# Performance work log

Measured on AMD Instinct MI355X. Metric: run time of the kernel, lower is better.

## Reference

```python
import jax, jax.numpy as jnp
import numpy as np

D_IN = 1024
D_OUT = 1024
N, S = 4, 2048

def setup_inputs() -> dict:
    key = jax.random.key(0)
    kv, kk, kq, k1, k2, k3 = jax.random.split(key, 6)
    return {
        "v": jax.random.normal(kv, (N, S, D_IN), dtype=jnp.float32),
        "k": jax.random.normal(kk, (N, S, D_IN), dtype=jnp.float32),
        "q": jax.random.normal(kq, (N, S, D_IN), dtype=jnp.float32),
        "WV": jax.random.normal(k1, (D_OUT, D_IN), dtype=jnp.float32),
        "WQ": jax.random.normal(k2, (D_OUT, D_IN), dtype=jnp.float32),
        "WK": jax.random.normal(k3, (D_OUT, D_IN), dtype=jnp.float32),
    }

def reference(v, k, q, WV, WQ, WK) -> jnp.ndarray:
    # projections: x @ W.T  -> [N, S, D_OUT]
    wv = jnp.einsum('nsw,ow->nso', v, WV)
    wk = jnp.einsum('nsw,ow->nso', k, WK)
    wq = jnp.einsum('nsw,ow->nso', q, WQ)
    # scores [N, Sq, Sk]; NOTE: softmax over axis=1 (query axis, matching torch dim=1),
    # then post-hoc division by input_shape[0] AFTER softmax (faithful to source).
    scores = jnp.einsum('nqo,nko->nqk', wq, wk)
    wqk = jax.nn.softmax(scores, axis=1) / jnp.float32(D_IN)
    return jnp.einsum('nqk,nko->nqo', wqk, wv)
```

## Files before the change

kernel.cpp:

```cpp
#include <hip/hip_runtime.h>
#include <math.h>


typedef _Float16 f16;
typedef _Float16 f16x8 __attribute__((ext_vector_type(8)));
typedef float f32x4 __attribute__((ext_vector_type(4)));

enum StageMode { SM_F32SPLIT, SM_F32HI, SM_PLANES2, SM_PLANES1, SM_EXP };
enum EpiMode   { EPI_F32, EPI_SPLIT, EPI_F16T };

#define PAD_PITCH 40
#define GLL_PITCH 32

__device__ __forceinline__ void gll16(const f16* g, f16* l) {
    __builtin_amdgcn_global_load_lds(
        (const __attribute__((address_space(1))) void*)g,
        (__attribute__((address_space(3))) void*)l, 16, 0, 0);
}

__device__ __forceinline__ void stage_gll_plane(const f16* __restrict__ gplane,
                                                f16* __restrict__ lds,
                                                long rowBase, int ld, int k0,
                                                int wave, int lane)
{
#pragma unroll
    for (int i = 0; i < 2; i++) {
        int slotBase = (wave * 2 + i) * 64;
        int t = slotBase + lane;
        int r = t >> 2;
        int c = (t & 3) ^ ((r >> 1) & 3);
        const f16* g = gplane + (rowBase + r) * (long)ld + k0 + c * 8;
        gll16(g, lds + (long)slotBase * 8);
    }
}

__device__ __forceinline__ int frag_off_gll(int row, int g) {
    return row * GLL_PITCH + ((g ^ ((row >> 1) & 3)) << 3);
}
__device__ __forceinline__ int frag_off_pad(int row, int g) {
    return row * PAD_PITCH + (g << 3);
}

template<StageMode SM>
__device__ __forceinline__ void stage_f32_tile(const float* __restrict__ gf,
                                               const float* __restrict__ pM,
                                               const float* __restrict__ pR,
                                               f16* __restrict__ Shi, f16* __restrict__ Slo,
                                               long rowBase, int ld, int k0, int tid)
{
#pragma unroll
    for (int i = 0; i < 2; i++) {
        int c  = tid + i * 256;
        int r  = c >> 2;
        int cc = c & 3;
        long g = (rowBase + r) * (long)ld + k0 + cc * 8;
        float4 x0 = *(const float4*)&gf[g];
        float4 x1 = *(const float4*)&gf[g + 4];
        float xs[8] = {x0.x, x0.y, x0.z, x0.w, x1.x, x1.y, x1.z, x1.w};
        if constexpr (SM == SM_EXP) {
            float4 ma = *(const float4*)&pM[k0 + cc * 8];
            float4 mb = *(const float4*)&pM[k0 + cc * 8 + 4];
            float4 ra = *(const float4*)&pR[k0 + cc * 8];
            float4 rb = *(const float4*)&pR[k0 + cc * 8 + 4];
            float ms[8] = {ma.x, ma.y, ma.z, ma.w, mb.x, mb.y, mb.z, mb.w};
            float rs[8] = {ra.x, ra.y, ra.z, ra.w, rb.x, rb.y, rb.z, rb.w};
            f16x8 h;
#pragma unroll
            for (int e = 0; e < 8; e++)
                h[e] = (f16)(__expf(xs[e] - ms[e]) * rs[e]);
            *(f16x8*)&Shi[r * PAD_PITCH + cc * 8] = h;
        } else if constexpr (SM == SM_F32HI) {
            f16x8 h;
#pragma unroll
            for (int e = 0; e < 8; e++) h[e] = (f16)xs[e];
            *(f16x8*)&Shi[r * PAD_PITCH + cc * 8] = h;
        } else {
            f16x8 h, l;
#pragma unroll
            for (int e = 0; e < 8; e++) {
                f16 hh = (f16)xs[e];
                h[e] = hh;
                l[e] = (f16)(xs[e] - (float)hh);
            }
            *(f16x8*)&Shi[r * PAD_PITCH + cc * 8] = h;
            *(f16x8*)&Slo[r * PAD_PITCH + cc * 8] = l;
        }
    }
}

template<StageMode SA, StageMode SB, EpiMode EP, int GROUPM, bool STATS>
__global__ __launch_bounds__(256, 4)
void mfma_gemm(const void* __restrict__ Ahi, const void* __restrict__ Alo,
               const void* __restrict__ Bhi, const void* __restrict__ Blo,
               const float* __restrict__ statM, const float* __restrict__ statR,
               float* __restrict__ pmOut, float* __restrict__ psOut,
               void* __restrict__ C0, void* __restrict__ C1,
               int M, int Nc, int K, int lda, int ldb, int ldc,
               long batchA, long batchB, long batchC,
               float epiScale, int tsShift)
{
    constexpr bool TRIPLE = (SA == SM_F32SPLIT || SA == SM_PLANES2);
    constexpr bool A_GLL  = (SA == SM_PLANES2 || SA == SM_PLANES1);
    constexpr bool B_GLL  = (SB == SM_PLANES2 || SB == SM_PLANES1);
    constexpr int A_SZ = A_GLL ? 128 * GLL_PITCH : 128 * PAD_PITCH;
    constexpr int B_SZ = B_GLL ? 128 * GLL_PITCH : 128 * PAD_PITCH;

    int bx, by;
    if constexpr (GROUPM > 0) {
        int gx = gridDim.x;
        int lin = blockIdx.y * gx + blockIdx.x;
        int nig = GROUPM * gx;
        int gid = lin / nig;
        int rem = lin - gid * nig;
        by = gid * GROUPM + (rem % GROUPM);
        bx = rem / GROUPM;
    } else {
        bx = blockIdx.x;
        by = blockIdx.y;
    }
    const int n0 = bx * 128;
    const int m0 = by * 128;
    const long z = blockIdx.z;

    long aOfs = z * batchA, bOfs = z * batchB, cOfs = z * batchC;
    const float* pM = statM + z * (long)K;
    const float* pR = statR + z * (long)K;

    __shared__ __align__(16) f16 As_hi[A_SZ];
    __shared__ __align__(16) f16 Bs_hi[B_SZ];
    __shared__ __align__(16) f16 As_lo[TRIPLE ? A_SZ : 8];
    __shared__ __align__(16) f16 Bs_lo[TRIPLE ? B_SZ : 8];

    const int tid  = threadIdx.x;
    const int lane = tid & 63;
    const int wave = tid >> 6;
    const int wr = (wave >> 1) * 64;
    const int wc = (wave & 1) * 64;
    const int fm = lane & 15;
    const int fg = lane >> 4;
    const int fk = fg * 8;

    f32x4 acc[4][4];
#pragma unroll
    for (int i = 0; i < 4; i++)
#pragma unroll
        for (int j = 0; j < 4; j++) acc[i][j] = (f32x4){0.f, 0.f, 0.f, 0.f};

    int roA[4], roB[4];
#pragma unroll
    for (int i = 0; i < 4; i++) {
        int rowA = wr + i * 16 + fm;
        int rowB = wc + i * 16 + fm;
        roA[i] = A_GLL ? frag_off_gll(rowA, fg) : frag_off_pad(rowA, fg);
        roB[i] = B_GLL ? frag_off_gll(rowB, fg) : frag_off_pad(rowB, fg);
    }

    for (int k0 = 0; k0 < K; k0 += 32) {
        if constexpr (SA == SM_PLANES2) {
            stage_gll_plane((const f16*)Ahi + aOfs, As_hi, m0, lda, k0, wave, lane);
            stage_gll_plane((const f16*)Alo + aOfs, As_lo, m0, lda, k0, wave, lane);
        } else if constexpr (SA == SM_PLANES1) {
            stage_gll_plane((const f16*)Ahi + aOfs, As_hi, m0, lda, k0, wave, lane);
        } else {
            stage_f32_tile<SA>((const float*)Ahi + aOfs, pM, pR, As_hi, As_lo, m0, lda, k0, tid);
        }
        if constexpr (SB == SM_PLANES2) {
            stage_gll_plane((const f16*)Bhi + bOfs, Bs_hi, n0, ldb, k0, wave, lane);
            stage_gll_plane((const f16*)Blo + bOfs, Bs_lo, n0, ldb, k0, wave, lane);
        } else if constexpr (SB == SM_PLANES1) {
            stage_gll_plane((const f16*)Bhi + bOfs, Bs_hi, n0, ldb, k0, wave, lane);
        } else {
            stage_f32_tile<SB>((const float*)Bhi + bOfs, nullptr, nullptr, Bs_hi, Bs_lo, n0, ldb, k0, tid);
        }
        __syncthreads();

        f16x8 ah[4], bh[4], al[4], bl[4];
#pragma unroll
        for (int i = 0; i < 4; i++) {
            ah[i] = *(const f16x8*)&As_hi[roA[i]];
            bh[i] = *(const f16x8*)&Bs_hi[roB[i]];
            if constexpr (TRIPLE) {
                al[i] = *(const f16x8*)&As_lo[roA[i]];
                bl[i] = *(const f16x8*)&Bs_lo[roB[i]];
            }
        }
#pragma unroll
        for (int i = 0; i < 4; i++) {
#pragma unroll
            for (int j = 0; j < 4; j++) {
                acc[i][j] = __builtin_amdgcn_mfma_f32_16x16x32_f16(ah[i], bh[j], acc[i][j], 0, 0, 0);
                if constexpr (TRIPLE) {
                    acc[i][j] = __builtin_amdgcn_mfma_f32_16x16x32_f16(ah[i], bl[j], acc[i][j], 0, 0, 0);
                    acc[i][j] = __builtin_amdgcn_mfma_f32_16x16x32_f16(al[i], bh[j], acc[i][j], 0, 0, 0);
                }
            }
        }
        __syncthreads();
    }

    const int cr = fg * 4;
    const int cn = fm;
#pragma unroll
    for (int i = 0; i < 4; i++) {
#pragma unroll
        for (int j = 0; j < 4; j++) {
#pragma unroll
            for (int r = 0; r < 4; r++) {
                long mg = m0 + wr + i * 16 + cr + r;
                long ng = n0 + wc + j * 16 + cn;
                float val = acc[i][j][r] * epiScale;
                if constexpr (EP == EPI_F32) {
                    ((float*)C0)[cOfs + mg * ldc + ng] = val;
                } else if constexpr (EP == EPI_SPLIT) {
                    f16 h = (f16)val;
                    ((f16*)C0)[cOfs + mg * ldc + ng] = h;
                    ((f16*)C1)[cOfs + mg * ldc + ng] = (f16)(val - (float)h);
                } else {
                    long TS = 1L << tsShift;
                    long nb = mg >> tsShift;
                    long s  = mg & (TS - 1);
                    long addr = nb * ((long)Nc << tsShift) + ng * TS + s;
                    ((f16*)C0)[addr] = (f16)val;
                }
            }
        }
    }

    if constexpr (STATS) {
        __shared__ float stM[2][128];
        __shared__ float stS[2][128];
#pragma unroll
        for (int j = 0; j < 4; j++) {
            float mj = -3.402823466e38f;
#pragma unroll
            for (int i = 0; i < 4; i++)
#pragma unroll
                for (int r = 0; r < 4; r++) mj = fmaxf(mj, acc[i][j][r]);
            float sj = 0.f;
#pragma unroll
            for (int i = 0; i < 4; i++)
#pragma unroll
                for (int r = 0; r < 4; r++) sj += __expf(acc[i][j][r] - mj);
#pragma unroll
            for (int mask = 16; mask <= 32; mask <<= 1) {
                float mo = __shfl_xor(mj, mask, 64);
                float so = __shfl_xor(sj, mask, 64);
                float mn = fmaxf(mj, mo);
                sj = sj * __expf(mj - mn) + so * __expf(mo - mn);
                mj = mn;
            }
            if (fg == 0) {
                stM[wave >> 1][wc + j * 16 + cn] = mj;
                stS[wave >> 1][wc + j * 16 + cn] = sj;
            }
        }
        __syncthreads();
        if (tid < 128) {
            float ma = stM[0][tid], mb = stM[1][tid];
            float Mc = fmaxf(ma, mb);
            float Sv = stS[0][tid] * __expf(ma - Mc) + stS[1][tid] * __expf(mb - Mc);
            long o = ((long)z * (M >> 7) + by) * (long)Nc + (long)bx * 128 + tid;
            pmOut[o] = Mc;
            psOut[o] = Sv;
        }
    }
}

__global__ __launch_bounds__(64)
void stats_combine_kernel(const float* __restrict__ pm, const float* __restrict__ ps,
                          float* __restrict__ statM, float* __restrict__ statR, int S)
{
    const int n = blockIdx.y;
    const int kk = blockIdx.x * 64 + threadIdx.x;
    float M = -INFINITY;
#pragma unroll
    for (int i = 0; i < 16; i++)
        M = fmaxf(M, pm[((long)n * 16 + i) * S + kk]);
    float Ssum = 0.f;
#pragma unroll
    for (int i = 0; i < 16; i++)
        Ssum += ps[((long)n * 16 + i) * S + kk] * __expf(pm[((long)n * 16 + i) * S + kk] - M);
    statM[(long)n * S + kk] = M;
    statR[(long)n * S + kk] = 1.0f / Ssum;
}

extern "C" void kernel_launch(void* const* d_in, const int* in_sizes, int n_in,
                              void* d_out, int out_size, void* d_ws, size_t ws_size,
                              hipStream_t stream)
{
    const float* v  = (const float*)d_in[0];
    const float* k  = (const float*)d_in[1];
    const float* q  = (const float*)d_in[2];
    const float* WV = (const float*)d_in[3];
    const float* WQ = (const float*)d_in[4];
    const float* WK = (const float*)d_in[5];
    float* out = (float*)d_out;

    const int N = 4, S = 2048, D = 1024;
    const long NSD = (long)N * S * D;
    const long NSS = (long)N * S * S;

    f16* ws = (f16*)d_ws;
    f16* wq_hi = ws;
    f16* wq_lo = ws + NSD;
    f16* wk_hi = ws + 2 * NSD;
    f16* wk_lo = ws + 3 * NSD;
    f16* wvT_hi = ws + 4 * NSD;
    float* Sc   = (float*)(ws + 5 * NSD);
    float* pm    = (float*)(ws + 9 * NSD);
    float* ps    = pm + (long)N * 16 * S;
    float* statM = ps + (long)N * 16 * S;
    float* statR = statM + (long)N * S;

    dim3 blk(256);

    {
        dim3 g(D / 128, (N * S) / 128, 1);
        mfma_gemm<SM_F32SPLIT, SM_F32SPLIT, EPI_SPLIT, 4, false><<<g, blk, 0, stream>>>(
            q, nullptr, WQ, nullptr, nullptr, nullptr, nullptr, nullptr, wq_hi, wq_lo,
            N * S, D, D, D, D, D, 0, 0, 0, 1.0f, 0);
        mfma_gemm<SM_F32SPLIT, SM_F32SPLIT, EPI_SPLIT, 4, false><<<g, blk, 0, stream>>>(
            k, nullptr, WK, nullptr, nullptr, nullptr, nullptr, nullptr, wk_hi, wk_lo,
            N * S, D, D, D, D, D, 0, 0, 0, 1.0f, 0);
        mfma_gemm<SM_F32HI, SM_F32HI, EPI_F16T, 4, false><<<g, blk, 0, stream>>>(
            v, nullptr, WV, nullptr, nullptr, nullptr, nullptr, nullptr, wvT_hi, nullptr,
            N * S, D, D, D, D, 0, 0, 0, 0, 1.0f, 11 );
    }
    {
        dim3 g(S / 128, S / 128, N);
        mfma_gemm<SM_PLANES2, SM_PLANES2, EPI_F32, 4, true><<<g, blk, 0, stream>>>(
            wq_hi, wq_lo, wk_hi, wk_lo, nullptr, nullptr, pm, ps, Sc, nullptr,
            S, S, D, D, D, S, (long)S * D, (long)S * D, (long)S * S, 1.0f, 0);
    }
    {
        dim3 gB(S / 64, N);
        stats_combine_kernel<<<gB, dim3(64), 0, stream>>>(pm, ps, statM, statR, S);
    }
    {
        dim3 g(D / 128, S / 128, N);
        mfma_gemm<SM_EXP, SM_PLANES1, EPI_F32, 0, false><<<g, blk, 0, stream>>>(
            Sc, nullptr, wvT_hi, nullptr, statM, statR, nullptr, nullptr, out, nullptr,
            S, D, S, S, S, D, (long)S * S, (long)S * D, (long)S * D, 1.0f / (float)D, 0);
    }
}
```

Measured before the change: 531.2 us.

## Pre-split inputs and softmax matrix to fp16 planes, stage all GEMMs via global_load_lds

Moves fp32-to-fp16 hi/lo splitting out of the GEMM inner loops into standalone elementwise kernels, and materializes the softmax probability matrix as fp16 in a separate pass. Every GEMM then stages tiles with direct global-to-LDS loads from half-precision planes, and the final GEMM gains grouped block ordering. This cuts per-tile conversion work, which was redone once per output column block, and halves the bytes the GEMMs read. The cost is extra kernel launches and extra memory round trips for the split planes and the P matrix, plus heavier reuse of workspace buffers.

```diff
diff --git a/kernel.cpp b/kernel.cpp
--- a/kernel.cpp
+++ b/kernel.cpp
@@ -4,12 +4,12 @@
 
 typedef _Float16 f16;
 typedef _Float16 f16x8 __attribute__((ext_vector_type(8)));
+typedef _Float16 f16x4 __attribute__((ext_vector_type(4)));
 typedef float f32x4 __attribute__((ext_vector_type(4)));
 
-enum StageMode { SM_F32SPLIT, SM_F32HI, SM_PLANES2, SM_PLANES1, SM_EXP };
+enum StageMode { SM_PLANES2, SM_PLANES1 };
 enum EpiMode   { EPI_F32, EPI_SPLIT, EPI_F16T };
 
-#define PAD_PITCH 40
 #define GLL_PITCH 32
 
 __device__ __forceinline__ void gll16(const f16* g, f16* l) {
@@ -37,73 +37,19 @@
 __device__ __forceinline__ int frag_off_gll(int row, int g) {
     return row * GLL_PITCH + ((g ^ ((row >> 1) & 3)) << 3);
 }
-__device__ __forceinline__ int frag_off_pad(int row, int g) {
-    return row * PAD_PITCH + (g << 3);
-}
-
-template<StageMode SM>
-__device__ __forceinline__ void stage_f32_tile(const float* __restrict__ gf,
-                                               const float* __restrict__ pM,
-                                               const float* __restrict__ pR,
-                                               f16* __restrict__ Shi, f16* __restrict__ Slo,
-                                               long rowBase, int ld, int k0, int tid)
-{
-#pragma unroll
-    for (int i = 0; i < 2; i++) {
-        int c  = tid + i * 256;
-        int r  = c >> 2;
-        int cc = c & 3;
-        long g = (rowBase + r) * (long)ld + k0 + cc * 8;
-        float4 x0 = *(const float4*)&gf[g];
-        float4 x1 = *(const float4*)&gf[g + 4];
-        float xs[8] = {x0.x, x0.y, x0.z, x0.w, x1.x, x1.y, x1.z, x1.w};
-        if constexpr (SM == SM_EXP) {
-            float4 ma = *(const float4*)&pM[k0 + cc * 8];
-            float4 mb = *(const float4*)&pM[k0 + cc * 8 + 4];
-            float4 ra = *(const float4*)&pR[k0 + cc * 8];
-            float4 rb = *(const float4*)&pR[k0 + cc * 8 + 4];
-            float ms[8] = {ma.x, ma.y, ma.z, ma.w, mb.x, mb.y, mb.z, mb.w};
-            float rs[8] = {ra.x, ra.y, ra.z, ra.w, rb.x, rb.y, rb.z, rb.w};
-            f16x8 h;
-#pragma unroll
-            for (int e = 0; e < 8; e++)
-                h[e] = (f16)(__expf(xs[e] - ms[e]) * rs[e]);
-            *(f16x8*)&Shi[r * PAD_PITCH + cc * 8] = h;
-        } else if constexpr (SM == SM_F32HI) {
-            f16x8 h;
-#pragma unroll
-            for (int e = 0; e < 8; e++) h[e] = (f16)xs[e];
-            *(f16x8*)&Shi[r * PAD_PITCH + cc * 8] = h;
-        } else {
-            f16x8 h, l;
-#pragma unroll
-            for (int e = 0; e < 8; e++) {
-                f16 hh = (f16)xs[e];
-                h[e] = hh;
-                l[e] = (f16)(xs[e] - (float)hh);
-            }
-            *(f16x8*)&Shi[r * PAD_PITCH + cc * 8] = h;
-            *(f16x8*)&Slo[r * PAD_PITCH + cc * 8] = l;
-        }
-    }
-}
 
 template<StageMode SA, StageMode SB, EpiMode EP, int GROUPM, bool STATS>
 __global__ __launch_bounds__(256, 4)
-void mfma_gemm(const void* __restrict__ Ahi, const void* __restrict__ Alo,
-               const void* __restrict__ Bhi, const void* __restrict__ Blo,
-               const float* __restrict__ statM, const float* __restrict__ statR,
+void mfma_gemm(const f16* __restrict__ Ahi, const f16* __restrict__ Alo,
+               const f16* __restrict__ Bhi, const f16* __restrict__ Blo,
                float* __restrict__ pmOut, float* __restrict__ psOut,
                void* __restrict__ C0, void* __restrict__ C1,
                int M, int Nc, int K, int lda, int ldb, int ldc,
                long batchA, long batchB, long batchC,
                float epiScale, int tsShift)
 {
-    constexpr bool TRIPLE = (SA == SM_F32SPLIT || SA == SM_PLANES2);
-    constexpr bool A_GLL  = (SA == SM_PLANES2 || SA == SM_PLANES1);
-    constexpr bool B_GLL  = (SB == SM_PLANES2 || SB == SM_PLANES1);
-    constexpr int A_SZ = A_GLL ? 128 * GLL_PITCH : 128 * PAD_PITCH;
-    constexpr int B_SZ = B_GLL ? 128 * GLL_PITCH : 128 * PAD_PITCH;
+    constexpr bool TRIPLE = (SA == SM_PLANES2);
+    constexpr int PLANE_SZ = 128 * GLL_PITCH;
 
     int bx, by;
     if constexpr (GROUPM > 0) {
@@ -122,14 +68,12 @@
     const int m0 = by * 128;
     const long z = blockIdx.z;
 
-    long aOfs = z * batchA, bOfs = z * batchB, cOfs = z * batchC;
-    const float* pM = statM + z * (long)K;
-    const float* pR = statR + z * (long)K;
-
-    __shared__ __align__(16) f16 As_hi[A_SZ];
-    __shared__ __align__(16) f16 Bs_hi[B_SZ];
-    __shared__ __align__(16) f16 As_lo[TRIPLE ? A_SZ : 8];
-    __shared__ __align__(16) f16 Bs_lo[TRIPLE ? B_SZ : 8];
+    const long aOfs = z * batchA, bOfs = z * batchB, cOfs = z * batchC;
+
+    __shared__ __align__(16) f16 As_hi[PLANE_SZ];
+    __shared__ __align__(16) f16 Bs_hi[PLANE_SZ];
+    __shared__ __align__(16) f16 As_lo[TRIPLE ? PLANE_SZ : 8];
+    __shared__ __align__(16) f16 Bs_lo[TRIPLE ? PLANE_SZ : 8];
 
     const int tid  = threadIdx.x;
     const int lane = tid & 63;
@@ -138,7 +82,6 @@
     const int wc = (wave & 1) * 64;
     const int fm = lane & 15;
     const int fg = lane >> 4;
-    const int fk = fg * 8;
 
     f32x4 acc[4][4];
 #pragma unroll
@@ -149,28 +92,16 @@
     int roA[4], roB[4];
 #pragma unroll
     for (int i = 0; i < 4; i++) {
-        int rowA = wr + i * 16 + fm;
-        int rowB = wc + i * 16 + fm;
-        roA[i] = A_GLL ? frag_off_gll(rowA, fg) : frag_off_pad(rowA, fg);
-        roB[i] = B_GLL ? frag_off_gll(rowB, fg) : frag_off_pad(rowB, fg);
+        roA[i] = frag_off_gll(wr + i * 16 + fm, fg);
+        roB[i] = frag_off_gll(wc + i * 16 + fm, fg);
     }
 
     for (int k0 = 0; k0 < K; k0 += 32) {
-        if constexpr (SA == SM_PLANES2) {
-            stage_gll_plane((const f16*)Ahi + aOfs, As_hi, m0, lda, k0, wave, lane);
-            stage_gll_plane((const f16*)Alo + aOfs, As_lo, m0, lda, k0, wave, lane);
-        } else if constexpr (SA == SM_PLANES1) {
-            stage_gll_plane((const f16*)Ahi + aOfs, As_hi, m0, lda, k0, wave, lane);
-        } else {
-            stage_f32_tile<SA>((const float*)Ahi + aOfs, pM, pR, As_hi, As_lo, m0, lda, k0, tid);
-        }
-        if constexpr (SB == SM_PLANES2) {
-            stage_gll_plane((const f16*)Bhi + bOfs, Bs_hi, n0, ldb, k0, wave, lane);
-            stage_gll_plane((const f16*)Blo + bOfs, Bs_lo, n0, ldb, k0, wave, lane);
-        } else if constexpr (SB == SM_PLANES1) {
-            stage_gll_plane((const f16*)Bhi + bOfs, Bs_hi, n0, ldb, k0, wave, lane);
-        } else {
-            stage_f32_tile<SB>((const float*)Bhi + bOfs, nullptr, nullptr, Bs_hi, Bs_lo, n0, ldb, k0, tid);
+        stage_gll_plane(Ahi + aOfs, As_hi, m0, lda, k0, wave, lane);
+        stage_gll_plane(Bhi + bOfs, Bs_hi, n0, ldb, k0, wave, lane);
+        if constexpr (TRIPLE) {
+            stage_gll_plane(Alo + aOfs, As_lo, m0, lda, k0, wave, lane);
+            stage_gll_plane(Blo + bOfs, Bs_lo, n0, ldb, k0, wave, lane);
         }
         __syncthreads();
 
@@ -266,6 +197,27 @@
     }
 }
 
+template<bool HAS_LO>
+__global__ __launch_bounds__(256)
+void split_kernel(const float* __restrict__ src, f16* __restrict__ hi,
+                  f16* __restrict__ lo, long n)
+{
+    long i = ((long)blockIdx.x * 256 + threadIdx.x) * 8;
+    if (i >= n) return;
+    float4 x0 = *(const float4*)&src[i];
+    float4 x1 = *(const float4*)&src[i + 4];
+    float xs[8] = {x0.x, x0.y, x0.z, x0.w, x1.x, x1.y, x1.z, x1.w};
+    f16x8 h, l;
+#pragma unroll
+    for (int e = 0; e < 8; e++) {
+        f16 hh = (f16)xs[e];
+        h[e] = hh;
+        if (HAS_LO) l[e] = (f16)(xs[e] - (float)hh);
+    }
+    *(f16x8*)&hi[i] = h;
+    if (HAS_LO) *(f16x8*)&lo[i] = l;
+}
+
 __global__ __launch_bounds__(64)
 void stats_combine_kernel(const float* __restrict__ pm, const float* __restrict__ ps,
                           float* __restrict__ statM, float* __restrict__ statR, int S)
@@ -282,6 +234,29 @@
         Ssum += ps[((long)n * 16 + i) * S + kk] * __expf(pm[((long)n * 16 + i) * S + kk] - M);
     statM[(long)n * S + kk] = M;
     statR[(long)n * S + kk] = 1.0f / Ssum;
+}
+
+__global__ __launch_bounds__(256)
+void pmat_kernel(const float* __restrict__ Sc, const float* __restrict__ statM,
+                 const float* __restrict__ statR, f16* __restrict__ Phi, int S)
+{
+    const int n = blockIdx.z;
+    const int kk = blockIdx.x * 1024 + threadIdx.x * 4;
+    const float* Sn = Sc + (long)n * S * S;
+    f16* ph = Phi + (long)n * S * S;
+    float4 M4 = *(const float4*)&statM[(long)n * S + kk];
+    float4 R4 = *(const float4*)&statR[(long)n * S + kk];
+    const int q0 = blockIdx.y * 32;
+    for (int qi = 0; qi < 32; qi++) {
+        long idx = (long)(q0 + qi) * S + kk;
+        float4 x = *(const float4*)&Sn[idx];
+        f16x4 p;
+        p[0] = (f16)(__expf(x.x - M4.x) * R4.x);
+        p[1] = (f16)(__expf(x.y - M4.y) * R4.y);
+        p[2] = (f16)(__expf(x.z - M4.z) * R4.z);
+        p[3] = (f16)(__expf(x.w - M4.w) * R4.w);
+        *(f16x4*)&ph[idx] = p;
+    }
 }
 
 extern "C" void kernel_launch(void* const* d_in, const int* in_sizes, int n_in,
@@ -298,38 +273,55 @@
 
     const int N = 4, S = 2048, D = 1024;
     const long NSD = (long)N * S * D;
-    const long NSS = (long)N * S * S;
+    const long DD  = (long)D * D;
 
     f16* ws = (f16*)d_ws;
-    f16* wq_hi = ws;
-    f16* wq_lo = ws + NSD;
-    f16* wk_hi = ws + 2 * NSD;
-    f16* wk_lo = ws + 3 * NSD;
-    f16* wvT_hi = ws + 4 * NSD;
-    float* Sc   = (float*)(ws + 5 * NSD);
-    float* pm    = (float*)(ws + 9 * NSD);
+    f16* q_hi = ws;
+    f16* q_lo = ws + NSD;
+    f16* k_hi = ws + 2 * NSD;
+    f16* k_lo = ws + 3 * NSD;
+    f16* v_hi = ws + 4 * NSD;
+    f16* Wb   = ws + 5 * NSD;
+    f16* WQ_hi = Wb,          *WQ_lo = Wb + DD;
+    f16* WK_hi = Wb + 2 * DD, *WK_lo = Wb + 3 * DD;
+    f16* WV_hi = Wb + 4 * DD;
+    f16* wq_hi = ws + 5 * NSD + 5 * DD;
+    f16* wq_lo = wq_hi + NSD;
+    f16* wk_hi = wq_hi + 2 * NSD;
+    f16* wk_lo = wq_hi + 3 * NSD;
+    f16* wvT_hi = ws;
+    float* Sc   = (float*)(ws + NSD);
+    f16* P_hi   = wq_hi;
+    float* pm    = (float*)(ws + 9 * NSD + 5 * DD);
     float* ps    = pm + (long)N * 16 * S;
     float* statM = ps + (long)N * 16 * S;
     float* statR = statM + (long)N * S;
 
     dim3 blk(256);
 
+    split_kernel<true ><<<dim3(NSD / 2048), blk, 0, stream>>>(q,  q_hi, q_lo, NSD);
+    split_kernel<true ><<<dim3(NSD / 2048), blk, 0, stream>>>(k,  k_hi, k_lo, NSD);
+    split_kernel<false><<<dim3(NSD / 2048), blk, 0, stream>>>(v,  v_hi, nullptr, NSD);
+    split_kernel<true ><<<dim3(DD / 2048),  blk, 0, stream>>>(WQ, WQ_hi, WQ_lo, DD);
+    split_kernel<true ><<<dim3(DD / 2048),  blk, 0, stream>>>(WK, WK_hi, WK_lo, DD);
+    split_kernel<false><<<dim3(DD / 2048),  blk, 0, stream>>>(WV, WV_hi, nullptr, DD);
+
     {
         dim3 g(D / 128, (N * S) / 128, 1);
-        mfma_gemm<SM_F32SPLIT, SM_F32SPLIT, EPI_SPLIT, 4, false><<<g, blk, 0, stream>>>(
-            q, nullptr, WQ, nullptr, nullptr, nullptr, nullptr, nullptr, wq_hi, wq_lo,
+        mfma_gemm<SM_PLANES2, SM_PLANES2, EPI_SPLIT, 4, false><<<g, blk, 0, stream>>>(
+            q_hi, q_lo, WQ_hi, WQ_lo, nullptr, nullptr, wq_hi, wq_lo,
             N * S, D, D, D, D, D, 0, 0, 0, 1.0f, 0);
-        mfma_gemm<SM_F32SPLIT, SM_F32SPLIT, EPI_SPLIT, 4, false><<<g, blk, 0, stream>>>(
-            k, nullptr, WK, nullptr, nullptr, nullptr, nullptr, nullptr, wk_hi, wk_lo,
+        mfma_gemm<SM_PLANES2, SM_PLANES2, EPI_SPLIT, 4, false><<<g, blk, 0, stream>>>(
+            k_hi, k_lo, WK_hi, WK_lo, nullptr, nullptr, wk_hi, wk_lo,
             N * S, D, D, D, D, D, 0, 0, 0, 1.0f, 0);
-        mfma_gemm<SM_F32HI, SM_F32HI, EPI_F16T, 4, false><<<g, blk, 0, stream>>>(
-            v, nullptr, WV, nullptr, nullptr, nullptr, nullptr, nullptr, wvT_hi, nullptr,
+        mfma_gemm<SM_PLANES1, SM_PLANES1, EPI_F16T, 4, false><<<g, blk, 0, stream>>>(
+            v_hi, nullptr, WV_hi, nullptr, nullptr, nullptr, wvT_hi, nullptr,
             N * S, D, D, D, D, 0, 0, 0, 0, 1.0f, 11 );
     }
     {
         dim3 g(S / 128, S / 128, N);
         mfma_gemm<SM_PLANES2, SM_PLANES2, EPI_F32, 4, true><<<g, blk, 0, stream>>>(
-            wq_hi, wq_lo, wk_hi, wk_lo, nullptr, nullptr, pm, ps, Sc, nullptr,
+            wq_hi, wq_lo, wk_hi, wk_lo, pm, ps, Sc, nullptr,
             S, S, D, D, D, S, (long)S * D, (long)S * D, (long)S * S, 1.0f, 0);
     }
     {
@@ -337,9 +329,13 @@
         stats_combine_kernel<<<gB, dim3(64), 0, stream>>>(pm, ps, statM, statR, S);
     }
     {
+        dim3 g(S / 1024, S / 32, N);
+        pmat_kernel<<<g, blk, 0, stream>>>(Sc, statM, statR, P_hi, S);
+    }
+    {
         dim3 g(D / 128, S / 128, N);
-        mfma_gemm<SM_EXP, SM_PLANES1, EPI_F32, 0, false><<<g, blk, 0, stream>>>(
-            Sc, nullptr, wvT_hi, nullptr, statM, statR, nullptr, nullptr, out, nullptr,
+        mfma_gemm<SM_PLANES1, SM_PLANES1, EPI_F32, 4, false><<<g, blk, 0, stream>>>(
+            P_hi, nullptr, wvT_hi, nullptr, nullptr, nullptr, out, nullptr,
             S, D, S, S, S, D, (long)S * S, (long)S * D, (long)S * D, 1.0f / (float)D, 0);
     }
 }
```

New measurement: 471.8 us. 11.2% less time.
